# Kernel optimization log

Measured on AMD Instinct MI355X. Metric: run time of the kernel, lower is better.

The kernel has to match this reference:

```python
import jax, jax.numpy as jnp
import numpy as np

D_MODEL = 1024
N_HEADS = 16
D_FF = 4096
B, T = 4, 2048
EPS = 1e-5


def layernorm(x, g, b):
    mu = jnp.mean(x, axis=-1, keepdims=True)
    var = jnp.var(x, axis=-1, keepdims=True)
    return (x - mu) * jax.lax.rsqrt(var + EPS) * g + b


def setup_inputs() -> dict:
    key = jax.random.key(0)
    ks = jax.random.split(key, 8)
    s = 0.02
    return {
        "x": jax.random.normal(ks[0], (B, T, D_MODEL), jnp.float32),
        "ln1_g": jnp.ones((D_MODEL,), jnp.float32),
        "ln1_b": jnp.zeros((D_MODEL,), jnp.float32),
        "wq": jax.random.normal(ks[1], (D_MODEL, D_MODEL), jnp.float32) * s,
        "bq": jnp.zeros((D_MODEL,), jnp.float32),
        "wk": jax.random.normal(ks[2], (D_MODEL, D_MODEL), jnp.float32) * s,
        "bk": jnp.zeros((D_MODEL,), jnp.float32),
        "wv": jax.random.normal(ks[3], (D_MODEL, D_MODEL), jnp.float32) * s,
        "bv": jnp.zeros((D_MODEL,), jnp.float32),
        "wo": jax.random.normal(ks[4], (D_MODEL, D_MODEL), jnp.float32) * s,
        "bo": jnp.zeros((D_MODEL,), jnp.float32),
        "ln2_g": jnp.ones((D_MODEL,), jnp.float32),
        "ln2_b": jnp.zeros((D_MODEL,), jnp.float32),
        "w1": jax.random.normal(ks[5], (D_FF, D_MODEL), jnp.float32) * s,
        "b1": jnp.zeros((D_FF,), jnp.float32),
        "w2": jax.random.normal(ks[6], (D_MODEL, D_FF), jnp.float32) * s,
        "b2": jnp.zeros((D_MODEL,), jnp.float32),
    }


def reference(x, ln1_g, ln1_b, wq, bq, wk, bk, wv, bv, wo, bo,
              ln2_g, ln2_b, w1, b1, w2, b2):
    d_k = D_MODEL // N_HEADS
    # --- attention sublayer (pre-LN) ---
    h = layernorm(x, ln1_g, ln1_b)                       # [B,T,D]
    q = (h @ wq.T + bq).reshape(B, T, N_HEADS, d_k)
    k = (h @ wk.T + bk).reshape(B, T, N_HEADS, d_k)
    v = (h @ wv.T + bv).reshape(B, T, N_HEADS, d_k)
    scores = jnp.einsum("bqhd,bkhd->bhqk", q, k) / jnp.sqrt(jnp.float32(d_k))
    attn = jax.nn.softmax(scores, axis=-1)               # [B,H,T,T]
    o = jnp.einsum("bhqk,bkhd->bqhd", attn, v).reshape(B, T, D_MODEL)
    x = x + (o @ wo.T + bo)
    # --- FFN sublayer ---
    h2 = layernorm(x, ln2_g, ln2_b)
    h2 = jax.nn.gelu(h2 @ w1.T + b1, approximate=False)  # torch GELU = exact erf
    x = x + (h2 @ w2.T + b2)
    return x
```

## Files before the change

kernel.cpp:

```cpp
#include <hip/hip_runtime.h>
#include <math.h>


#define D_MODEL 1024
#define D_FF    4096
#define NH      16
#define BATCH   4
#define SEQ     2048
#define DK      64
#define MTOK    (BATCH*SEQ)
#define NBH     (BATCH*NH)

typedef __bf16 bf16;
typedef _Float16 f16;
typedef bf16  bf16x4 __attribute__((ext_vector_type(4)));
typedef bf16  bf16x8 __attribute__((ext_vector_type(8)));
typedef f16   f16x4  __attribute__((ext_vector_type(4)));
typedef f16   f16x8  __attribute__((ext_vector_type(8)));
typedef __fp16 hf16x2 __attribute__((ext_vector_type(2)));
typedef __fp16 hf16x4 __attribute__((ext_vector_type(4)));
typedef __fp16 hf16x8 __attribute__((ext_vector_type(8)));
typedef float f32x4  __attribute__((ext_vector_type(4)));

__device__ __forceinline__ void gload_lds16(const void* g, void* l) {
  __builtin_amdgcn_global_load_lds(
      (__attribute__((address_space(1))) void*)g,
      (__attribute__((address_space(3))) void*)l, 16, 0, 0);
}

#define BAR() __builtin_amdgcn_s_barrier()
#define WAIT_VM0() do { asm volatile("s_waitcnt vmcnt(0)" ::: "memory"); \
  __builtin_amdgcn_sched_barrier(0); } while (0)

__device__ __forceinline__ float gelu_fast(float x) {
  float ax = fabsf(x) * 0.70710678118654752f;
  float t  = 1.0f / (1.0f + 0.3275911f * ax);
  float p  = t * (0.254829592f + t * (-0.284496736f + t * (1.421413741f +
             t * (-1.453152027f + t * 1.061405429f))));
  float e  = __builtin_amdgcn_exp2f(ax * ax * -1.4426950408889634f);
  float er = 1.0f - p * e;
  er = __builtin_copysignf(er, x);
  return 0.5f * x * (1.0f + er);
}

__global__ __launch_bounds__(256) void cast_w(const float* __restrict__ s,
                                              bf16* __restrict__ d, int n) {
  int i = (blockIdx.x * 256 + threadIdx.x) * 4;
  if (i >= n) return;
  float4 v = *(const float4*)(s + i);
  bf16x4 o;
  o[0] = (bf16)v.x; o[1] = (bf16)v.y; o[2] = (bf16)v.z; o[3] = (bf16)v.w;
  *(bf16x4*)(d + i) = o;
}

__global__ __launch_bounds__(256) void ln_kernel(const float* __restrict__ x,
                                                 const float* __restrict__ g,
                                                 const float* __restrict__ b,
                                                 bf16* __restrict__ out) {
  int row = blockIdx.x;
  int tid = threadIdx.x;
  const float* xr = x + (size_t)row * D_MODEL;
  float4 v = *(const float4*)(xr + tid * 4);
  float s  = v.x + v.y + v.z + v.w;
  float sq = v.x*v.x + v.y*v.y + v.z*v.z + v.w*v.w;
  #pragma unroll
  for (int off = 1; off < 64; off <<= 1) {
    s  += __shfl_xor(s,  off, 64);
    sq += __shfl_xor(sq, off, 64);
  }
  __shared__ float ls[4], lq[4];
  int wid = tid >> 6, lane = tid & 63;
  if (lane == 0) { ls[wid] = s; lq[wid] = sq; }
  __syncthreads();
  s  = ls[0] + ls[1] + ls[2] + ls[3];
  sq = lq[0] + lq[1] + lq[2] + lq[3];
  float mu   = s * (1.0f / D_MODEL);
  float var  = sq * (1.0f / D_MODEL) - mu * mu;
  float rstd = rsqrtf(var + 1e-5f);
  float4 gv = *(const float4*)(g + tid * 4);
  float4 bv = *(const float4*)(b + tid * 4);
  bf16x4 o;
  o[0] = (bf16)((v.x - mu) * rstd * gv.x + bv.x);
  o[1] = (bf16)((v.y - mu) * rstd * gv.y + bv.y);
  o[2] = (bf16)((v.z - mu) * rstd * gv.z + bv.z);
  o[3] = (bf16)((v.w - mu) * rstd * gv.w + bv.w);
  *(bf16x4*)(out + (size_t)row * D_MODEL + tid * 4) = o;
}

enum { EP_QKV = 0, EP_RESID = 1, EP_GELU = 2 };

#define QSCALE 0.18033688011112042f

template <int EP, int CFG>
__global__ __launch_bounds__(512) void gemm8p(
    const bf16* __restrict__ A, const bf16* __restrict__ W,
    const float* __restrict__ bias,
    const float* __restrict__ resid,
    float* __restrict__ out_f32,
    bf16* __restrict__ out_bf,
    int M, int N, int K) {
  constexpr int BM  = CFG ? 128 : 256;
  constexpr int BK  = CFG ? 64 : 32;
  constexpr int WM  = CFG ? 64 : 128;
  constexpr int FRN = WM / 16;
  constexpr int KKN = BK / 32;
  constexpr int RB  = BK * 2;
  constexpr int GR  = RB / 16;
  constexpr int RSH = CFG ? 7 : 6;
  constexpr int AB  = 16384;
  constexpr int TB  = AB + 256 * BK * 2;
  constexpr int L   = TB / 8192;
  constexpr int NBUF = CFG ? 3 : 4;
  constexpr int PD   = NBUF - 1;

  __shared__ char lds[NBUF * TB];

  int tiles_n = N >> 8;
  int nwg = (M / BM) * tiles_n;
  int bid = blockIdx.x;
  int swz = (bid & 7) * (nwg >> 3) + (bid >> 3);
  int bm = swz / tiles_n, bn = swz % tiles_n;
  int m0 = bm * BM, n0 = bn << 8;
  int tid = threadIdx.x, wid = tid >> 6, lane = tid & 63;
  int wm = wid >> 2, wn = wid & 3;
  int l15 = lane & 15, l4 = lane >> 4;

  f32x4 acc[FRN][4];
  #pragma unroll
  for (int i = 0; i < FRN; i++)
    #pragma unroll
    for (int j = 0; j < 4; j++)
      #pragma unroll
      for (int e = 0; e < 4; e++) acc[i][j][e] = 0.f;

  auto STAGE = [&](int kt, int nb) {
    char* buf = lds + nb * TB;
    #pragma unroll
    for (int l = 0; l < L; ++l) {
      bool isA = l < 2;
      int o = (isA ? l : l - 2) * 8192 + tid * 16;
      int row = o >> RSH;
      int g = (o >> 4) & (GR - 1);
      int gs = g ^ (CFG ? (row & 7) : ((row >> 1) & 3));
      const bf16* src = (isA ? A + (size_t)(m0 + row) * K
                             : W + (size_t)(n0 + row) * K) + kt * BK + gs * 8;
      gload_lds16(src, buf + (isA ? 0 : AB) + o);
    }
  };

  int nt = K / BK;
  STAGE(0, 0);
  STAGE(1, 1);
  if constexpr (CFG == 0) {
    STAGE(2, 2);
    asm volatile("s_waitcnt vmcnt(8)" ::: "memory");
  } else {
    asm volatile("s_waitcnt vmcnt(6)" ::: "memory");
  }
  __builtin_amdgcn_sched_barrier(0);
  BAR();

  for (int t = 0; t < nt; ++t) {
    const char* bc = lds + (t % NBUF) * TB;

    if (t + PD < nt) STAGE(t + PD, (t + PD) % NBUF);

    bf16x8 af[FRN][KKN], bfr[4][KKN];
    #pragma unroll
    for (int f = 0; f < FRN; ++f)
      #pragma unroll
      for (int kk = 0; kk < KKN; ++kk) {
        int row = wm * WM + f * 16 + l15;
        int g = (kk * 4 + l4) ^ (CFG ? (row & 7) : ((row >> 1) & 3));
        af[f][kk] = *(const bf16x8*)(bc + row * RB + g * 16);
      }
    #pragma unroll
    for (int fc = 0; fc < 4; ++fc)
      #pragma unroll
      for (int kk = 0; kk < KKN; ++kk) {
        int row = wn * 64 + fc * 16 + l15;
        int g = (kk * 4 + l4) ^ (CFG ? (row & 7) : ((row >> 1) & 3));
        bfr[fc][kk] = *(const bf16x8*)(bc + AB + row * RB + g * 16);
      }

    __builtin_amdgcn_s_setprio(1);
    #pragma unroll
    for (int f = 0; f < FRN; ++f)
      #pragma unroll
      for (int fc = 0; fc < 4; ++fc)
        #pragma unroll
        for (int kk = 0; kk < KKN; ++kk)
          acc[f][fc] = __builtin_amdgcn_mfma_f32_16x16x32_bf16(af[f][kk], bfr[fc][kk],
                                                               acc[f][fc], 0, 0, 0);
    __builtin_amdgcn_s_setprio(0);

    if constexpr (CFG == 0) {
      if (t + 3 < nt)      { asm volatile("s_waitcnt vmcnt(8)" ::: "memory"); }
      else if (t + 2 < nt) { asm volatile("s_waitcnt vmcnt(4)" ::: "memory"); }
      else if (t + 1 < nt) { asm volatile("s_waitcnt vmcnt(0)" ::: "memory"); }
    } else {
      if (t + 2 < nt)      { asm volatile("s_waitcnt vmcnt(6)" ::: "memory"); }
      else if (t + 1 < nt) { asm volatile("s_waitcnt vmcnt(0)" ::: "memory"); }
    }
    __builtin_amdgcn_sched_barrier(0);
    BAR();
  }

  if (EP == EP_QKV) {
    #pragma unroll
    for (int i = 0; i < FRN; i++)
      #pragma unroll
      for (int j = 0; j < 4; j++) {
        int gm0 = m0 + wm * WM + i * 16 + (l4 << 2);
        int gn  = n0 + wn * 64 + j * 16 + l15;
        int which = gn >> 10;
        int nn = gn & 1023, head = nn >> 6, d = nn & 63;
        int bb = gm0 >> 11, t = gm0 & 2047;
        float bv = bias[gn];
        if (which == 2) {
          int sbase = (t & ~31) + ((t >> 2) & 3) * 8 + ((t >> 4) & 1) * 4;
          f16x4 pk;
          #pragma unroll
          for (int jj = 0; jj < 4; jj++) pk[jj] = (f16)(acc[i][j][jj] + bv);
          *(f16x4*)((f16*)out_bf + (size_t)2 * NBH * SEQ * DK +
                    ((size_t)(bb * NH + head) * DK + d) * SEQ + sbase) = pk;
        } else {
          float scale = (which == 0) ? QSCALE : 1.0f;
          #pragma unroll
          for (int jj = 0; jj < 4; jj++) {
            float cv = (acc[i][j][jj] + bv) * scale;
            size_t idx = (size_t)which * (NBH * SEQ * DK) +
                         ((size_t)(bb * NH + head) * SEQ + (t + jj)) * DK + d;
            out_bf[idx] = (bf16)cv;
          }
        }
      }
  } else {
    #pragma unroll
    for (int i = 0; i < FRN; i++)
      #pragma unroll
      for (int j = 0; j < 4; j++)
        #pragma unroll
        for (int jj = 0; jj < 4; jj++) {
          int gm = m0 + wm * WM + i * 16 + (l4 << 2) + jj;
          int gn = n0 + wn * 64 + j * 16 + l15;
          float cv = acc[i][j][jj] + bias[gn];
          if (EP == EP_RESID) {
            size_t idx = (size_t)gm * N + gn;
            out_f32[idx] = resid[idx] + cv;
          } else {
            out_bf[(size_t)gm * N + gn] = (bf16)gelu_fast(cv);
          }
        }
  }
}

__global__ __launch_bounds__(512) void attn_kernel(
    const bf16* __restrict__ q, const bf16* __restrict__ k,
    const f16* __restrict__ vt, bf16* __restrict__ o) {
  __shared__ bf16 kt_lds[2][64 * 64];
  __shared__ f16  vt_lds[2][64 * 64];
  int bid = blockIdx.x;
  int swzb = (bid & 7) * 128 + (bid >> 3);
  int bh = swzb >> 4;
  int qt = swzb & 15;
  int t0 = qt << 7;
  int tid = threadIdx.x, wid = tid >> 6, lane = tid & 63;
  int l15 = lane & 15, l4 = lane >> 4;

  int kb0 = l15 * 128 + ((l4 ^ (l15 & 7)) << 4);
  int kb1 = l15 * 128 + (((4 + l4) ^ (l15 & 7)) << 4);
  int vb32[2];
  #pragma unroll
  for (int n = 0; n < 2; n++)
    vb32[n] = l15 * 128 + (((n * 4 + l4) ^ (l15 & 7)) << 4);

  const bf16* qbase = q + ((size_t)bh * SEQ + t0 + wid * 16 + l15) * DK;
  bf16x8 qf[2];
  qf[0] = *(const bf16x8*)(qbase + (l4 << 3));
  qf[1] = *(const bf16x8*)(qbase + 32 + (l4 << 3));

  f16x8 vones8;
  #pragma unroll
  for (int e = 0; e < 8; e++) vones8[e] = (f16)1.f;
  float m_run = -1e30f;
  f32x4 acc_o[4];
  f32x4 acc_l;
  #pragma unroll
  for (int nd = 0; nd < 4; nd++)
    #pragma unroll
    for (int e = 0; e < 4; e++) acc_o[nd][e] = 0.f;
  #pragma unroll
  for (int e = 0; e < 4; e++) acc_l[e] = 0.f;

  int oK = tid * 16;
  int rowk = oK >> 7, gk = (oK >> 4) & 7;
  const bf16* gKsrc = k + ((size_t)bh * SEQ + rowk) * DK + ((gk ^ (rowk & 7)) << 3);
  int dV = oK >> 7, gd = (oK >> 4) & 7;
  const f16* gVsrc = vt + ((size_t)bh * DK + dV) * SEQ + ((gd ^ (dV & 7)) << 3);

  auto stage = [&](int buf, int t) {
    int kv0 = t * 64;
    gload_lds16(gKsrc + (size_t)kv0 * DK, (char*)&kt_lds[buf][0] + tid * 16);
    gload_lds16(gVsrc + kv0, (char*)&vt_lds[buf][0] + tid * 16);
  };

  stage(0, 0);
  WAIT_VM0();
  BAR();

  for (int t = 0; t < SEQ / 64; ++t) {
    int cur = t & 1;
    if (t < SEQ / 64 - 1) stage(cur ^ 1, t + 1);
    const char* kbase = (const char*)&kt_lds[cur][0];
    const char* vbase = (const char*)&vt_lds[cur][0];

    f32x4 accs[4];
    #pragma unroll
    for (int n = 0; n < 4; n++)
      #pragma unroll
      for (int e = 0; e < 4; e++) accs[n][e] = 0.f;
    __builtin_amdgcn_s_setprio(1);
    #pragma unroll
    for (int n = 0; n < 4; n++) {
      bf16x8 kf0 = *(const bf16x8*)(kbase + kb0 + n * 2048);
      bf16x8 kf1 = *(const bf16x8*)(kbase + kb1 + n * 2048);
      accs[n] = __builtin_amdgcn_mfma_f32_16x16x32_bf16(kf0, qf[0], accs[n], 0, 0, 0);
      accs[n] = __builtin_amdgcn_mfma_f32_16x16x32_bf16(kf1, qf[1], accs[n], 0, 0, 0);
    }
    __builtin_amdgcn_s_setprio(0);

    float mloc = -1e30f;
    #pragma unroll
    for (int n = 0; n < 4; n++) {
      float a0 = fmaxf(accs[n][0], accs[n][1]);
      float a1 = fmaxf(accs[n][2], accs[n][3]);
      mloc = fmaxf(mloc, fmaxf(a0, a1));
    }
    float mt = fmaxf(mloc, __shfl_xor(mloc, 16, 64));
    mt = fmaxf(mt, __shfl_xor(mt, 32, 64));
    if (__any(mt > m_run + 8.0f)) {
      float mn = fmaxf(m_run, mt);
      float sc = __builtin_amdgcn_exp2f(m_run - mn);
      m_run = mn;
      float scr0 = __shfl(sc, l4 * 20 + 0, 64);
      float scr1 = __shfl(sc, l4 * 20 + 1, 64);
      float scr2 = __shfl(sc, l4 * 20 + 2, 64);
      float scr3 = __shfl(sc, l4 * 20 + 3, 64);
      #pragma unroll
      for (int nd = 0; nd < 4; nd++) {
        acc_o[nd][0] *= scr0; acc_o[nd][1] *= scr1;
        acc_o[nd][2] *= scr2; acc_o[nd][3] *= scr3;
      }
      acc_l[0] *= scr0; acc_l[1] *= scr1; acc_l[2] *= scr2; acc_l[3] *= scr3;
    }
    f16x8 pa32[2];
    #pragma unroll
    for (int n = 0; n < 2; n++) {
      float e0 = __builtin_amdgcn_exp2f(accs[2*n][0] - m_run);
      float e1 = __builtin_amdgcn_exp2f(accs[2*n][1] - m_run);
      float e2 = __builtin_amdgcn_exp2f(accs[2*n][2] - m_run);
      float e3 = __builtin_amdgcn_exp2f(accs[2*n][3] - m_run);
      float e4 = __builtin_amdgcn_exp2f(accs[2*n+1][0] - m_run);
      float e5 = __builtin_amdgcn_exp2f(accs[2*n+1][1] - m_run);
      float e6 = __builtin_amdgcn_exp2f(accs[2*n+1][2] - m_run);
      float e7 = __builtin_amdgcn_exp2f(accs[2*n+1][3] - m_run);
      hf16x2 p01 = __builtin_amdgcn_cvt_pkrtz(e0, e1);
      hf16x2 p23 = __builtin_amdgcn_cvt_pkrtz(e2, e3);
      hf16x2 p45 = __builtin_amdgcn_cvt_pkrtz(e4, e5);
      hf16x2 p67 = __builtin_amdgcn_cvt_pkrtz(e6, e7);
      hf16x4 lo = __builtin_shufflevector(p01, p23, 0, 1, 2, 3);
      hf16x4 hi = __builtin_shufflevector(p45, p67, 0, 1, 2, 3);
      hf16x8 cmb = __builtin_shufflevector(lo, hi, 0, 1, 2, 3, 4, 5, 6, 7);
      pa32[n] = __builtin_bit_cast(f16x8, cmb);
    }

    __builtin_amdgcn_s_setprio(1);
    #pragma unroll
    for (int n = 0; n < 2; n++) {
      #pragma unroll
      for (int nd = 0; nd < 4; nd++) {
        f16x8 vf = *(const f16x8*)(vbase + vb32[n] + nd * 2048);
        acc_o[nd] = __builtin_amdgcn_mfma_f32_16x16x32_f16(pa32[n], vf, acc_o[nd], 0, 0, 0);
      }
      acc_l = __builtin_amdgcn_mfma_f32_16x16x32_f16(pa32[n], vones8, acc_l, 0, 0, 0);
    }
    __builtin_amdgcn_s_setprio(0);

    if (t < SEQ / 64 - 1) { WAIT_VM0(); }
    BAR();
  }

  float rl0 = 1.0f / acc_l[0], rl1 = 1.0f / acc_l[1];
  float rl2 = 1.0f / acc_l[2], rl3 = 1.0f / acc_l[3];
  int bb = bh >> 4, hh = bh & 15;
  #pragma unroll
  for (int nd = 0; nd < 4; nd++) {
    int d = nd * 16 + l15;
    int rowb = t0 + wid * 16 + l4 * 4;
    o[((size_t)bb * SEQ + rowb + 0) * D_MODEL + hh * DK + d] = (bf16)(acc_o[nd][0] * rl0);
    o[((size_t)bb * SEQ + rowb + 1) * D_MODEL + hh * DK + d] = (bf16)(acc_o[nd][1] * rl1);
    o[((size_t)bb * SEQ + rowb + 2) * D_MODEL + hh * DK + d] = (bf16)(acc_o[nd][2] * rl2);
    o[((size_t)bb * SEQ + rowb + 3) * D_MODEL + hh * DK + d] = (bf16)(acc_o[nd][3] * rl3);
  }
}

extern "C" void kernel_launch(void* const* d_in, const int* in_sizes, int n_in,
                              void* d_out, int out_size, void* d_ws, size_t ws_size,
                              hipStream_t stream) {
  const float* x    = (const float*)d_in[0];
  const float* ln1g = (const float*)d_in[1];
  const float* ln1b = (const float*)d_in[2];
  const float* wq   = (const float*)d_in[3];
  const float* bq   = (const float*)d_in[4];
  const float* wk   = (const float*)d_in[5];
  const float* bk   = (const float*)d_in[6];
  const float* wv   = (const float*)d_in[7];
  const float* bv   = (const float*)d_in[8];
  const float* wo   = (const float*)d_in[9];
  const float* bo   = (const float*)d_in[10];
  const float* ln2g = (const float*)d_in[11];
  const float* ln2b = (const float*)d_in[12];
  const float* w1   = (const float*)d_in[13];
  const float* b1   = (const float*)d_in[14];
  const float* w2   = (const float*)d_in[15];
  const float* b2   = (const float*)d_in[16];
  float* out = (float*)d_out;

  char* ws = (char*)d_ws;
  bf16* wqkv_b = (bf16*)(ws);
  bf16* wo_b   = (bf16*)(ws + ((size_t)6  << 20));
  bf16* w1_b   = (bf16*)(ws + ((size_t)8  << 20));
  bf16* w2_b   = (bf16*)(ws + ((size_t)16 << 20));
  bf16* h_b    = (bf16*)(ws + ((size_t)24 << 20));
  bf16* qkv_b  = (bf16*)(ws + ((size_t)40 << 20));
  bf16* o_b    = (bf16*)(ws + ((size_t)88 << 20));
  bf16* ffn1_b = (bf16*)(ws + ((size_t)40 << 20));
  float* bqkv  = (float*)(ws + ((size_t)104 << 20));

  cast_w<<<1024, 256, 0, stream>>>(wq, wqkv_b, 1 << 20);
  cast_w<<<1024, 256, 0, stream>>>(wk, wqkv_b + (1 << 20), 1 << 20);
  cast_w<<<1024, 256, 0, stream>>>(wv, wqkv_b + (2 << 20), 1 << 20);
  cast_w<<<1024, 256, 0, stream>>>(wo, wo_b, 1 << 20);
  cast_w<<<4096, 256, 0, stream>>>(w1, w1_b, 1 << 22);
  cast_w<<<4096, 256, 0, stream>>>(w2, w2_b, 1 << 22);
  (void)hipMemcpyAsync(bqkv,        bq, 4096, hipMemcpyDeviceToDevice, stream);
  (void)hipMemcpyAsync(bqkv + 1024, bk, 4096, hipMemcpyDeviceToDevice, stream);
  (void)hipMemcpyAsync(bqkv + 2048, bv, 4096, hipMemcpyDeviceToDevice, stream);

  ln_kernel<<<MTOK, 256, 0, stream>>>(x, ln1g, ln1b, h_b);
  gemm8p<EP_QKV, 1><<<768, 512, 0, stream>>>(h_b, wqkv_b, bqkv, nullptr, nullptr,
                                             qkv_b, MTOK, 3072, 1024);
  attn_kernel<<<NBH * 16, 512, 0, stream>>>(qkv_b, qkv_b + (size_t)NBH * SEQ * DK,
                                            (const f16*)(qkv_b + (size_t)2 * NBH * SEQ * DK),
                                            o_b);
  gemm8p<EP_RESID, 1><<<256, 512, 0, stream>>>(o_b, wo_b, bo, x, out, nullptr,
                                               MTOK, 1024, 1024);
  ln_kernel<<<MTOK, 256, 0, stream>>>(out, ln2g, ln2b, h_b);
  gemm8p<EP_GELU, 0><<<512, 512, 0, stream>>>(h_b, w1_b, b1, nullptr, nullptr,
                                              ffn1_b, MTOK, 4096, 1024);
  gemm8p<EP_RESID, 1><<<256, 512, 0, stream>>>(ffn1_b, w2_b, b2, out, out, nullptr,
                                               MTOK, 1024, 4096);
}
```

Before: 413.3 us.

## Load attention V directly to registers and use triple-buffered GEMM pipeline

```diff
diff --git a/kernel.cpp b/kernel.cpp
--- a/kernel.cpp
+++ b/kernel.cpp
@@ -110,10 +110,8 @@
   constexpr int AB  = 16384;
   constexpr int TB  = AB + 256 * BK * 2;
   constexpr int L   = TB / 8192;
-  constexpr int NBUF = CFG ? 3 : 4;
-  constexpr int PD   = NBUF - 1;
-
-  __shared__ char lds[NBUF * TB];
+
+  __shared__ char lds[3 * TB];
 
   int tiles_n = N >> 8;
   int nwg = (M / BM) * tiles_n;
@@ -151,19 +149,16 @@
   int nt = K / BK;
   STAGE(0, 0);
   STAGE(1, 1);
-  if constexpr (CFG == 0) {
-    STAGE(2, 2);
-    asm volatile("s_waitcnt vmcnt(8)" ::: "memory");
-  } else {
-    asm volatile("s_waitcnt vmcnt(6)" ::: "memory");
-  }
+  if constexpr (CFG) { asm volatile("s_waitcnt vmcnt(6)" ::: "memory"); }
+  else               { asm volatile("s_waitcnt vmcnt(4)" ::: "memory"); }
   __builtin_amdgcn_sched_barrier(0);
   BAR();
 
   for (int t = 0; t < nt; ++t) {
-    const char* bc = lds + (t % NBUF) * TB;
-
-    if (t + PD < nt) STAGE(t + PD, (t + PD) % NBUF);
+    int cb = t % 3, nb = cb >= 1 ? cb - 1 : 2;
+    const char* bc = lds + cb * TB;
+
+    if (t + 2 < nt) STAGE(t + 2, nb);
 
     bf16x8 af[FRN][KKN], bfr[4][KKN];
     #pragma unroll
@@ -194,15 +189,13 @@
                                                                acc[f][fc], 0, 0, 0);
     __builtin_amdgcn_s_setprio(0);
 
-    if constexpr (CFG == 0) {
-      if (t + 3 < nt)      { asm volatile("s_waitcnt vmcnt(8)" ::: "memory"); }
-      else if (t + 2 < nt) { asm volatile("s_waitcnt vmcnt(4)" ::: "memory"); }
-      else if (t + 1 < nt) { asm volatile("s_waitcnt vmcnt(0)" ::: "memory"); }
-    } else {
-      if (t + 2 < nt)      { asm volatile("s_waitcnt vmcnt(6)" ::: "memory"); }
-      else if (t + 1 < nt) { asm volatile("s_waitcnt vmcnt(0)" ::: "memory"); }
-    }
-    __builtin_amdgcn_sched_barrier(0);
+    if (t + 2 < nt) {
+      if constexpr (CFG) { asm volatile("s_waitcnt vmcnt(6)" ::: "memory"); }
+      else               { asm volatile("s_waitcnt vmcnt(4)" ::: "memory"); }
+      __builtin_amdgcn_sched_barrier(0);
+    } else if (t + 1 < nt) {
+      WAIT_VM0();
+    }
     BAR();
   }
 
@@ -259,7 +252,6 @@
     const bf16* __restrict__ q, const bf16* __restrict__ k,
     const f16* __restrict__ vt, bf16* __restrict__ o) {
   __shared__ bf16 kt_lds[2][64 * 64];
-  __shared__ f16  vt_lds[2][64 * 64];
   int bid = blockIdx.x;
   int swzb = (bid & 7) * 128 + (bid >> 3);
   int bh = swzb >> 4;
@@ -270,10 +262,7 @@
 
   int kb0 = l15 * 128 + ((l4 ^ (l15 & 7)) << 4);
   int kb1 = l15 * 128 + (((4 + l4) ^ (l15 & 7)) << 4);
-  int vb32[2];
-  #pragma unroll
-  for (int n = 0; n < 2; n++)
-    vb32[n] = l15 * 128 + (((n * 4 + l4) ^ (l15 & 7)) << 4);
+  const f16* vgbase = vt + ((size_t)bh * DK + l15) * SEQ + l4 * 8;
 
   const bf16* qbase = q + ((size_t)bh * SEQ + t0 + wid * 16 + l15) * DK;
   bf16x8 qf[2];
@@ -296,24 +285,28 @@
   int oK = tid * 16;
   int rowk = oK >> 7, gk = (oK >> 4) & 7;
   const bf16* gKsrc = k + ((size_t)bh * SEQ + rowk) * DK + ((gk ^ (rowk & 7)) << 3);
-  int dV = oK >> 7, gd = (oK >> 4) & 7;
-  const f16* gVsrc = vt + ((size_t)bh * DK + dV) * SEQ + ((gd ^ (dV & 7)) << 3);
-
-  auto stage = [&](int buf, int t) {
-    int kv0 = t * 64;
-    gload_lds16(gKsrc + (size_t)kv0 * DK, (char*)&kt_lds[buf][0] + tid * 16);
-    gload_lds16(gVsrc + kv0, (char*)&vt_lds[buf][0] + tid * 16);
+
+  auto stageK = [&](int buf, int t) {
+    gload_lds16(gKsrc + (size_t)(t * 64) * DK, (char*)&kt_lds[buf][0] + tid * 16);
   };
 
-  stage(0, 0);
+  stageK(0, 0);
   WAIT_VM0();
   BAR();
 
   for (int t = 0; t < SEQ / 64; ++t) {
     int cur = t & 1;
-    if (t < SEQ / 64 - 1) stage(cur ^ 1, t + 1);
+    int kv0 = t * 64;
+
+    f16x8 vreg[2][4];
+    #pragma unroll
+    for (int n = 0; n < 2; n++)
+      #pragma unroll
+      for (int nd = 0; nd < 4; nd++)
+        vreg[n][nd] = *(const f16x8*)(vgbase + (size_t)nd * 16 * SEQ + kv0 + n * 32);
+
+    if (t < SEQ / 64 - 1) stageK(cur ^ 1, t + 1);
     const char* kbase = (const char*)&kt_lds[cur][0];
-    const char* vbase = (const char*)&vt_lds[cur][0];
 
     f32x4 accs[4];
     #pragma unroll
@@ -379,10 +372,8 @@
     #pragma unroll
     for (int n = 0; n < 2; n++) {
       #pragma unroll
-      for (int nd = 0; nd < 4; nd++) {
-        f16x8 vf = *(const f16x8*)(vbase + vb32[n] + nd * 2048);
-        acc_o[nd] = __builtin_amdgcn_mfma_f32_16x16x32_f16(pa32[n], vf, acc_o[nd], 0, 0, 0);
-      }
+      for (int nd = 0; nd < 4; nd++)
+        acc_o[nd] = __builtin_amdgcn_mfma_f32_16x16x32_f16(pa32[n], vreg[n][nd], acc_o[nd], 0, 0, 0);
       acc_l = __builtin_amdgcn_mfma_f32_16x16x32_f16(pa32[n], vones8, acc_l, 0, 0, 0);
     }
     __builtin_amdgcn_s_setprio(0);
```

Measured after the change: 556.5 us. +34.6%, slower.
